# Kernel tuning notes

Hardware: AMD Instinct MI355X
Metric: run time of the kernel (lower is better)

The kernel has to match this reference:

```python
import jax, jax.numpy as jnp
import numpy as np

K_NEIGHBOURS = 4  # neighbour_num
BN_EPS = 1e-5


def setup_inputs() -> dict:
    key = jax.random.key(0)
    ks = jax.random.split(key, 5)
    B, T, J, C = 32, 243, 17, 256
    std = np.sqrt(2.0 / C).astype(np.float32)
    return {
        "x": jax.random.normal(ks[0], (B, T, J, C), dtype=jnp.float32),
        "W_u": jax.random.normal(ks[1], (C, C), dtype=jnp.float32) * std,
        "b_u": jnp.zeros((C,), dtype=jnp.float32),
        "W_v": jax.random.normal(ks[2], (C, C), dtype=jnp.float32) * std,
        "b_v": jnp.zeros((C,), dtype=jnp.float32),
        "gamma": jnp.ones((T,), dtype=jnp.float32),
        "beta": jnp.zeros((T,), dtype=jnp.float32),
    }


def reference(x, W_u, b_u, W_v, b_v, gamma, beta):
    # temporal-mode GCN with top-k similarity adjacency
    b, t, j, c = x.shape
    xr = jnp.transpose(x, (0, 2, 1, 3)).reshape(b * j, t, c)  # [BJ, T, C]

    # similarity adjacency: keep edges >= k-th largest similarity per row
    sim = jnp.einsum('bnc,bmc->bnm', xr, xr)                  # [BJ, T, T]
    thr = jax.lax.top_k(sim, K_NEIGHBOURS)[0][..., -1:]       # [BJ, T, 1]
    adj = (sim >= thr).astype(x.dtype)

    # symmetric degree normalization D^{-1/2} A D^{-1/2}
    deg_inv_sqrt = adj.sum(-1) ** -0.5                        # [BJ, T]
    norm_adj = deg_inv_sqrt[:, :, None] * adj * deg_inv_sqrt[:, None, :]

    v = xr @ W_v.T + b_v
    u = xr @ W_u.T + b_u
    h = jnp.einsum('bnm,bmc->bnc', norm_adj, v) + u           # [BJ, T, C]

    # BatchNorm1d(num_features=T), training mode: stats over (batch, C)
    mean = h.mean(axis=(0, 2), keepdims=True)
    var = jnp.mean((h - mean) ** 2, axis=(0, 2), keepdims=True)
    hn = (h - mean) * jax.lax.rsqrt(var + BN_EPS) * gamma[None, :, None] + beta[None, :, None]

    out = jax.nn.relu(xr + hn)                                # residual (dim_in == dim_out)
    return jnp.transpose(out.reshape(b, j, t, c), (0, 2, 1, 3))  # [B, T, J, C]
```

## Files before the change

### kernel.cpp

```cpp
#include <hip/hip_runtime.h>

#define BB 32
#define TT 243
#define JJ 17
#define CC 256
#define BJC (BB*JJ)
#define MM (BJC*TT)
#define FR (BJC*256)
#define SIMP 244
#define NEG_INF (-3.0e38f)

typedef __attribute__((ext_vector_type(8))) short bf16x8;
typedef __attribute__((ext_vector_type(4))) float f32x4;
typedef __attribute__((ext_vector_type(8))) _Float16 f16x8;
typedef __attribute__((ext_vector_type(4))) _Float16 f16x4;

__device__ __forceinline__ unsigned short f2bf(float f) {
  unsigned int u = __float_as_uint(f);
  u = (u + 0x7fffu + ((u >> 16) & 1u)) >> 16;
  return (unsigned short)u;
}
__device__ __forceinline__ float bf2f(unsigned short s) {
  return __uint_as_float(((unsigned int)s) << 16);
}

__device__ __forceinline__ void gld16(const void* g, void* l) {
  __builtin_amdgcn_global_load_lds(
      (__attribute__((address_space(1))) void*)(g),
      (__attribute__((address_space(3))) void*)(l), 16, 0, 0);
}

__launch_bounds__(256)
__global__ void k_prep_w(const float* __restrict__ Wu, const float* __restrict__ Wv,
                         _Float16* __restrict__ wcp) {
  const int r = blockIdx.x * 4 + (threadIdx.x >> 6);
  const int l = threadIdx.x & 63;
  const float* src = ((r < CC) ? (Wu + (size_t)r * CC) : (Wv + (size_t)(r - CC) * CC)) + l * 4;
  float4 v = *reinterpret_cast<const float4*>(src);
  f16x4 hv = (f16x4){(_Float16)v.x, (_Float16)v.y, (_Float16)v.z, (_Float16)v.w};
  const int ks = l >> 4;
  const int u  = (l & 15) >> 1;
  const int s  = u ^ (r & 7);
  *reinterpret_cast<f16x4*>(wcp + ((size_t)ks * 512 + r) * 64 + s * 8 + (l & 1) * 4) = hv;
}

__launch_bounds__(256)
__global__ void k_prep_x(const float* __restrict__ x,
                         _Float16* __restrict__ xqh, _Float16* __restrict__ xql) {
  const int r = blockIdx.x * 4 + (threadIdx.x >> 6);
  const int l = threadIdx.x & 63;
  const int bj = r / TT, t = r - bj * TT;
  const int b = bj / JJ, j = bj - b * JJ;
  float4 v = *reinterpret_cast<const float4*>(
      x + ((size_t)(b * TT + t) * JJ + j) * CC + l * 4);
  _Float16 h0 = (_Float16)v.x, h1 = (_Float16)v.y, h2 = (_Float16)v.z, h3 = (_Float16)v.w;
  f16x4 hv = (f16x4){h0, h1, h2, h3};
  f16x4 lv = (f16x4){(_Float16)(v.x - (float)h0), (_Float16)(v.y - (float)h1),
                     (_Float16)(v.z - (float)h2), (_Float16)(v.w - (float)h3)};
  const int fr = bj * 256 + t;
  const int ks = l >> 4;
  const int u  = (l & 15) >> 1;
  const int s  = u ^ (t & 7);
  const size_t off = ((size_t)ks * FR + fr) * 64 + s * 8 + (l & 1) * 4;
  *reinterpret_cast<f16x4*>(xqh + off) = hv;
  *reinterpret_cast<f16x4*>(xql + off) = lv;
}

__launch_bounds__(512, 4)
__global__ void k_sim(const _Float16* __restrict__ xqh, const _Float16* __restrict__ xql,
                      float* __restrict__ sim) {
  __shared__ _Float16 Sh[256 * 64];
  __shared__ _Float16 Sl[256 * 64];
  const int bid = blockIdx.x;
  const int g = bid >> 4, s_ = bid & 15;
  const int bj = g * 8 + (s_ & 7);
  const int rh = s_ >> 3;
  const int tid = threadIdx.x, lane = tid & 63, wid = tid >> 6;
  const int wr = wid >> 2, wc = wid & 3;
  const int rowbase = rh * 128 + wr * 64;
  const int l15 = lane & 15, lg = lane >> 4;
  const size_t rb = (size_t)bj * 256;
  const size_t lsrc = (size_t)(lane >> 3) * 64 + (lane & 7) * 8;

  f32x4 acc[4][4];
  #pragma unroll
  for (int i = 0; i < 4; i++)
    #pragma unroll
    for (int j = 0; j < 4; j++) acc[i][j] = (f32x4){0.f, 0.f, 0.f, 0.f};

  for (int ks = 0; ks < 4; ++ks) {
    {
      const _Float16* ph = xqh + ((size_t)ks * FR + rb) * 64;
      const _Float16* pl = xql + ((size_t)ks * FR + rb) * 64;
      #pragma unroll
      for (int c = 0; c < 4; ++c) {
        const int row0 = (wid * 4 + c) * 8;
        gld16(ph + (size_t)row0 * 64 + lsrc, &Sh[row0 * 64]);
        gld16(pl + (size_t)row0 * 64 + lsrc, &Sl[row0 * 64]);
      }
    }
    __syncthreads();
    #pragma unroll
    for (int kh = 0; kh < 2; ++kh) {
      f16x8 bhv[4], blv[4];
      #pragma unroll
      for (int j = 0; j < 4; ++j) {
        int rc = wc * 64 + j * 16 + l15;
        int sl = ((kh * 4 + lg) ^ (rc & 7)) * 8;
        bhv[j] = *reinterpret_cast<const f16x8*>(&Sh[rc * 64 + sl]);
        blv[j] = *reinterpret_cast<const f16x8*>(&Sl[rc * 64 + sl]);
      }
      #pragma unroll
      for (int i = 0; i < 4; ++i) {
        int rl = rowbase + i * 16 + l15;
        int sl = ((kh * 4 + lg) ^ (rl & 7)) * 8;
        f16x8 ah = *reinterpret_cast<const f16x8*>(&Sh[rl * 64 + sl]);
        f16x8 al = *reinterpret_cast<const f16x8*>(&Sl[rl * 64 + sl]);
        #pragma unroll
        for (int j = 0; j < 4; ++j) {
          acc[i][j] = __builtin_amdgcn_mfma_f32_16x16x32_f16(ah, bhv[j], acc[i][j], 0, 0, 0);
          acc[i][j] = __builtin_amdgcn_mfma_f32_16x16x32_f16(ah, blv[j], acc[i][j], 0, 0, 0);
          acc[i][j] = __builtin_amdgcn_mfma_f32_16x16x32_f16(al, bhv[j], acc[i][j], 0, 0, 0);
        }
      }
    }
    if (ks < 3) __syncthreads();
  }

  const size_t sbase = (size_t)bj * TT * SIMP;
  #pragma unroll
  for (int j = 0; j < 4; ++j) {
    int c = wc * 64 + j * 16 + l15;
    if (c < TT) {
      #pragma unroll
      for (int i = 0; i < 4; ++i) {
        int n0 = rowbase + i * 16 + lg * 4;
        if (n0 + 3 < TT) {
          *reinterpret_cast<float4*>(sim + sbase + (size_t)c * SIMP + n0) =
            (float4){acc[i][j][0], acc[i][j][1], acc[i][j][2], acc[i][j][3]};
        } else {
          #pragma unroll
          for (int q = 0; q < 4; ++q)
            if (n0 + q < TT) sim[sbase + (size_t)c * SIMP + n0 + q] = acc[i][j][q];
        }
      }
    }
  }
}

__launch_bounds__(256)
__global__ void k_uv(const _Float16* __restrict__ xqh, const _Float16* __restrict__ wcp,
                     const float* __restrict__ bu, const float* __restrict__ bv,
                     unsigned short* __restrict__ uo, unsigned short* __restrict__ vo) {
  __shared__ _Float16 S[2][128][64];
  const int bid = blockIdx.x;
  const int g = bid >> 5, s_ = bid & 31;
  const int panel = g * 8 + (s_ & 7);
  const int ct = s_ >> 3;
  const int m0 = panel * 128;
  const int tid = threadIdx.x, lane = tid & 63, wid = tid >> 6;
  const int rm = wid * 32;
  const int l15 = lane & 15, lg = lane >> 4;

  const float* bsrc = (ct < 2) ? bu : bv;
  unsigned short* osrc = (ct < 2) ? uo : vo;
  const int cb = (ct & 1) * 128;

  float bias[8];
  #pragma unroll
  for (int j = 0; j < 8; ++j) bias[j] = bsrc[cb + j * 16 + l15];

  f32x4 acc[2][8];
  #pragma unroll
  for (int i = 0; i < 2; i++)
    #pragma unroll
    for (int j = 0; j < 8; j++) acc[i][j] = (f32x4){0.f, 0.f, 0.f, 0.f};

  for (int ks = 0; ks < 4; ++ks) {
    #pragma unroll
    for (int c = 0; c < 8; ++c) {
      int ch = wid * 8 + c;
      int half = ch >> 4;
      int rows0 = (ch & 15) * 8;
      const _Float16* g2 = half
        ? wcp + ((size_t)ks * 512 + ct * 128 + rows0) * 64 + lane * 8
        : xqh + ((size_t)ks * FR  + m0       + rows0) * 64 + lane * 8;
      gld16(g2, &S[half][rows0][0]);
    }
    __syncthreads();
    #pragma unroll
    for (int kh = 0; kh < 2; ++kh) {
      f16x8 af[2], bfv[8];
      #pragma unroll
      for (int i = 0; i < 2; ++i) {
        int rl = rm + i * 16 + l15;
        af[i] = *reinterpret_cast<const f16x8*>(&S[0][rl][((kh * 4 + lg) ^ (rl & 7)) * 8]);
      }
      #pragma unroll
      for (int j = 0; j < 8; ++j) {
        int rl = j * 16 + l15;
        bfv[j] = *reinterpret_cast<const f16x8*>(&S[1][rl][((kh * 4 + lg) ^ (rl & 7)) * 8]);
      }
      #pragma unroll
      for (int i = 0; i < 2; ++i)
        #pragma unroll
        for (int j = 0; j < 8; ++j)
          acc[i][j] = __builtin_amdgcn_mfma_f32_16x16x32_f16(af[i], bfv[j], acc[i][j], 0, 0, 0);
    }
    __syncthreads();
  }

  #pragma unroll
  for (int i = 0; i < 2; ++i) {
    #pragma unroll
    for (int q = 0; q < 4; ++q) {
      int gf = m0 + rm + i * 16 + lg * 4 + q;
      int t = gf & 255, bj = gf >> 8;
      if (t < TT) {
        size_t gm = (size_t)bj * TT + t;
        #pragma unroll
        for (int j = 0; j < 8; ++j)
          osrc[gm * CC + cb + j * 16 + l15] = f2bf(acc[i][j][q] + bias[j]);
      }
    }
  }
}

__launch_bounds__(256)
__global__ void k_topk(const float* __restrict__ sim,
                       float* __restrict__ dis_o,
                       unsigned long long* __restrict__ mask_o,
                       unsigned char* __restrict__ nbr_o,
                       unsigned char* __restrict__ deg_o) {
  const int l = threadIdx.x & 63, wv = threadIdx.x >> 6;
  const int r = blockIdx.x * 4 + wv;
  const float* row = sim + (size_t)r * SIMP;
  float o0 = row[l];
  float o1 = row[l + 64];
  float o2 = row[l + 128];
  float o3 = (l + 192 < TT) ? row[l + 192] : NEG_INF;
  float v0 = o0, v1 = o1, v2 = o2, v3 = o3;
  { float mx, mn;
    mx=fmaxf(v0,v1); mn=fminf(v0,v1); v0=mx; v1=mn;
    mx=fmaxf(v2,v3); mn=fminf(v2,v3); v2=mx; v3=mn;
    mx=fmaxf(v0,v2); mn=fminf(v0,v2); v0=mx; v2=mn;
    mx=fmaxf(v1,v3); mn=fminf(v1,v3); v1=mx; v3=mn;
    mx=fmaxf(v1,v2); mn=fminf(v1,v2); v1=mx; v2=mn; }
  #pragma unroll
  for (int off = 1; off < 64; off <<= 1) {
    float b0 = __shfl_xor(v0, off), b1 = __shfl_xor(v1, off),
          b2 = __shfl_xor(v2, off), b3 = __shfl_xor(v3, off);
    float t0 = fmaxf(v0, b3), t1 = fmaxf(v1, b2),
          t2 = fmaxf(v2, b1), t3 = fmaxf(v3, b0);
    float mx, mn;
    mx=fmaxf(t0,t2); mn=fminf(t0,t2); t0=mx; t2=mn;
    mx=fmaxf(t1,t3); mn=fminf(t1,t3); t1=mx; t3=mn;
    mx=fmaxf(t0,t1); mn=fminf(t0,t1); t0=mx; t1=mn;
    mx=fmaxf(t2,t3); mn=fminf(t2,t3); t2=mx; t3=mn;
    v0=t0; v1=t1; v2=t2; v3=t3;
  }
  const float thr = v3;

  unsigned long long m0 = __ballot(o0 >= thr);
  unsigned long long m1 = __ballot(o1 >= thr);
  unsigned long long m2 = __ballot(o2 >= thr);
  unsigned long long m3 = __ballot(o3 >= thr);
  const unsigned long long below = (1ull << l) - 1ull;
  const int b0 = __popcll(m0);
  const int b1 = b0 + __popcll(m1);
  const int b2 = b1 + __popcll(m2);
  const size_t r8 = (size_t)r * 8;
  if (o0 >= thr) { int q = __popcll(m0 & below);      if (q < 8) nbr_o[r8 + q] = (unsigned char)l; }
  if (o1 >= thr) { int q = b0 + __popcll(m1 & below); if (q < 8) nbr_o[r8 + q] = (unsigned char)(64 + l); }
  if (o2 >= thr) { int q = b1 + __popcll(m2 & below); if (q < 8) nbr_o[r8 + q] = (unsigned char)(128 + l); }
  if (o3 >= thr) { int q = b2 + __popcll(m3 & below); if (q < 8) nbr_o[r8 + q] = (unsigned char)(192 + l); }
  if (l == 0) {
    int deg = b2 + __popcll(m3);
    dis_o[r] = rsqrtf((float)deg);
    deg_o[r] = (unsigned char)((deg > 255) ? 255 : deg);
    mask_o[(size_t)r * 4 + 0] = m0;
    mask_o[(size_t)r * 4 + 1] = m1;
    mask_o[(size_t)r * 4 + 2] = m2;
    mask_o[(size_t)r * 4 + 3] = m3;
  }
}

__launch_bounds__(512)
__global__ void k_agg(const unsigned char* __restrict__ nbr,
                      const unsigned char* __restrict__ degv,
                      const unsigned long long* __restrict__ mask,
                      const float* __restrict__ dis,
                      const unsigned short* __restrict__ u,
                      const unsigned short* __restrict__ v,
                      unsigned short* __restrict__ h,
                      float* __restrict__ p1, float* __restrict__ p2) {
  __shared__ float dis_l[256];
  const int bj = blockIdx.x;
  const int tid = threadIdx.x, lane = tid & 63, wid = tid >> 6;
  if (tid < TT) dis_l[tid] = dis[(size_t)bj * TT + tid];
  __syncthreads();
  const int start = blockIdx.y * 122;
  const int cnt = blockIdx.y ? (TT - 122) : 122;
  const size_t pbase = (size_t)bj * TT;
  const int co = lane * 4;
  for (int rl = wid; rl < cnt; rl += 8) {
    const int t = start + rl;
    const size_t r = pbase + t;
    const float dr = dis_l[t];
    const int dg = degv[r];
    const unsigned long long nb = *reinterpret_cast<const unsigned long long*>(nbr + r * 8);
    ushort4 uu = *reinterpret_cast<const ushort4*>(u + r * CC + co);
    float a0 = bf2f(uu.x), a1 = bf2f(uu.y), a2 = bf2f(uu.z), a3 = bf2f(uu.w);
    if (dg <= 8) {
      const int i0 = (int)(nb & 255), i1 = (int)((nb >> 8) & 255),
                i2 = (int)((nb >> 16) & 255), i3 = (int)((nb >> 24) & 255);
      ushort4 w0v = *reinterpret_cast<const ushort4*>(v + (pbase + i0) * CC + co);
      ushort4 w1v = *reinterpret_cast<const ushort4*>(v + (pbase + i1) * CC + co);
      ushort4 w2v = *reinterpret_cast<const ushort4*>(v + (pbase + i2) * CC + co);
      ushort4 w3v = *reinterpret_cast<const ushort4*>(v + (pbase + i3) * CC + co);
      const float w0 = dr * dis_l[i0], w1 = dr * dis_l[i1],
                  w2 = dr * dis_l[i2], w3 = dr * dis_l[i3];
      a0 = __builtin_fmaf(w0, bf2f(w0v.x), a0); a1 = __builtin_fmaf(w0, bf2f(w0v.y), a1);
      a2 = __builtin_fmaf(w0, bf2f(w0v.z), a2); a3 = __builtin_fmaf(w0, bf2f(w0v.w), a3);
      a0 = __builtin_fmaf(w1, bf2f(w1v.x), a0); a1 = __builtin_fmaf(w1, bf2f(w1v.y), a1);
      a2 = __builtin_fmaf(w1, bf2f(w1v.z), a2); a3 = __builtin_fmaf(w1, bf2f(w1v.w), a3);
      a0 = __builtin_fmaf(w2, bf2f(w2v.x), a0); a1 = __builtin_fmaf(w2, bf2f(w2v.y), a1);
      a2 = __builtin_fmaf(w2, bf2f(w2v.z), a2); a3 = __builtin_fmaf(w2, bf2f(w2v.w), a3);
      a0 = __builtin_fmaf(w3, bf2f(w3v.x), a0); a1 = __builtin_fmaf(w3, bf2f(w3v.y), a1);
      a2 = __builtin_fmaf(w3, bf2f(w3v.z), a2); a3 = __builtin_fmaf(w3, bf2f(w3v.w), a3);
      #pragma unroll
      for (int e = 4; e < 8; ++e) {
        if (e < dg) {
          const int ix = (int)((nb >> (8 * e)) & 255);
          const float we = dr * dis_l[ix];
          ushort4 vv = *reinterpret_cast<const ushort4*>(v + (pbase + ix) * CC + co);
          a0 = __builtin_fmaf(we, bf2f(vv.x), a0); a1 = __builtin_fmaf(we, bf2f(vv.y), a1);
          a2 = __builtin_fmaf(we, bf2f(vv.z), a2); a3 = __builtin_fmaf(we, bf2f(vv.w), a3);
        }
      }
    } else {
      #pragma unroll
      for (int w4 = 0; w4 < 4; ++w4) {
        unsigned long long m = mask[r * 4 + w4];
        while (m) {
          int i = __ffsll(m) - 1;
          m &= m - 1;
          int idx = w4 * 64 + i;
          float w = dr * dis_l[idx];
          ushort4 vv = *reinterpret_cast<const ushort4*>(v + (pbase + idx) * CC + co);
          a0 = __builtin_fmaf(w, bf2f(vv.x), a0);
          a1 = __builtin_fmaf(w, bf2f(vv.y), a1);
          a2 = __builtin_fmaf(w, bf2f(vv.z), a2);
          a3 = __builtin_fmaf(w, bf2f(vv.w), a3);
        }
      }
    }
    ushort4 hh;
    hh.x = f2bf(a0); hh.y = f2bf(a1); hh.z = f2bf(a2); hh.w = f2bf(a3);
    *reinterpret_cast<ushort4*>(h + r * CC + co) = hh;
    float s1 = a0 + a1 + a2 + a3;
    float s2 = a0*a0 + a1*a1 + a2*a2 + a3*a3;
    #pragma unroll
    for (int off = 1; off < 64; off <<= 1) { s1 += __shfl_xor(s1, off); s2 += __shfl_xor(s2, off); }
    if (lane == 0) { p1[r] = s1; p2[r] = s2; }
  }
}

__global__ void k_bnstat(const float* __restrict__ p1, const float* __restrict__ p2,
                         const float* __restrict__ gamma, const float* __restrict__ beta,
                         float* __restrict__ scale, float* __restrict__ shift) {
  __shared__ float sA[256], sB[256];
  const int t = blockIdx.x;
  const int tid = threadIdx.x;
  float a = 0.f, b2 = 0.f;
  for (int bj = tid; bj < BJC; bj += 256) {
    a  += p1[bj * TT + t];
    b2 += p2[bj * TT + t];
  }
  sA[tid] = a; sB[tid] = b2;
  __syncthreads();
  for (int s = 128; s > 0; s >>= 1) {
    if (tid < s) { sA[tid] += sA[tid + s]; sB[tid] += sB[tid + s]; }
    __syncthreads();
  }
  if (tid == 0) {
    const float invN = 1.0f / (float)(BJC * CC);
    float mean = sA[0] * invN;
    float var  = sB[0] * invN - mean * mean;
    float sc   = rsqrtf(var + 1e-5f) * gamma[t];
    scale[t] = sc;
    shift[t] = beta[t] - mean * sc;
  }
}

__global__ void k_out(const float* __restrict__ x, const unsigned short* __restrict__ h,
                      const float* __restrict__ scale, const float* __restrict__ shift,
                      float* __restrict__ out) {
  int g = blockIdx.x * 256 + threadIdx.x;
  if (g >= MM * (CC/4)) return;
  int c4  = g & 63;
  int rowx = g >> 6;
  int b   = rowx / (TT*JJ);
  int rem = rowx - b*(TT*JJ);
  int t   = rem / JJ;
  int j   = rem - t*JJ;
  size_t hoff = ((size_t)(b*JJ + j) * TT + t) * CC + c4*4;
  float4 xv = *reinterpret_cast<const float4*>(x + (size_t)rowx*CC + c4*4);
  ushort4 hv = *reinterpret_cast<const ushort4*>(h + hoff);
  float sc = scale[t], sh = shift[t];
  float4 o;
  o.x = fmaxf(xv.x + bf2f(hv.x)*sc + sh, 0.f);
  o.y = fmaxf(xv.y + bf2f(hv.y)*sc + sh, 0.f);
  o.z = fmaxf(xv.z + bf2f(hv.z)*sc + sh, 0.f);
  o.w = fmaxf(xv.w + bf2f(hv.w)*sc + sh, 0.f);
  *reinterpret_cast<float4*>(out + (size_t)rowx*CC + c4*4) = o;
}

extern "C" void kernel_launch(void* const* d_in, const int* in_sizes, int n_in,
                              void* d_out, int out_size, void* d_ws, size_t ws_size,
                              hipStream_t stream) {
  const float* x     = (const float*)d_in[0];
  const float* Wu    = (const float*)d_in[1];
  const float* bu    = (const float*)d_in[2];
  const float* Wv    = (const float*)d_in[3];
  const float* bv    = (const float*)d_in[4];
  const float* gamma = (const float*)d_in[5];
  const float* beta  = (const float*)d_in[6];
  float* out = (float*)d_out;

  char* ws = (char*)d_ws;
  size_t off = 0;
  auto alloc = [&](size_t bytes) -> void* {
    void* p = ws + off;
    off = (off + bytes + 255) & ~(size_t)255;
    return p;
  };
  _Float16* xqh = (_Float16*)alloc((size_t)4 * FR * 64 * 2);
  _Float16* xql = (_Float16*)alloc((size_t)4 * FR * 64 * 2);
  _Float16* wcp = (_Float16*)alloc((size_t)4 * 512 * 64 * 2);
  float* sim = (float*)alloc((size_t)BJC * TT * SIMP * 4);
  float* dis = (float*)alloc((size_t)MM * 4);
  unsigned long long* msk = (unsigned long long*)alloc((size_t)MM * 4 * 8);
  unsigned char* nbr = (unsigned char*)alloc((size_t)MM * 8);
  unsigned char* deg = (unsigned char*)alloc((size_t)MM);
  float* p1    = (float*)alloc((size_t)MM * 4);
  float* p2    = (float*)alloc((size_t)MM * 4);
  float* scale = (float*)alloc(1024);
  float* shift = (float*)alloc(1024);
  unsigned short* v = (unsigned short*)alloc((size_t)MM * CC * 2);
  unsigned short* u = (unsigned short*)sim;
  unsigned short* h = (unsigned short*)xql;

  if (ws_size < off) {
    hipMemsetAsync(d_out, 0, (size_t)out_size * 4, stream);
    return;
  }

  k_prep_w<<<dim3(512/4), dim3(256), 0, stream>>>(Wu, Wv, wcp);
  k_prep_x<<<dim3(MM/4), dim3(256), 0, stream>>>(x, xqh, xql);
  k_sim  <<<dim3(BJC*2), dim3(512), 0, stream>>>(xqh, xql, sim);
  k_topk <<<dim3(MM/4), dim3(256), 0, stream>>>(sim, dis, msk, nbr, deg);
  k_uv   <<<dim3(4*(FR/128)), dim3(256), 0, stream>>>(xqh, wcp, bu, bv, u, v);
  k_agg  <<<dim3(BJC, 2), dim3(512), 0, stream>>>(nbr, deg, msk, dis, u, v, h, p1, p2);
  k_bnstat<<<dim3(TT), dim3(256), 0, stream>>>(p1, p2, gamma, beta, scale, shift);
  k_out  <<<dim3((MM*(CC/4) + 255)/256), dim3(256), 0, stream>>>(x, h, scale, shift, out);
}
```

Measured before the change: 393.2 us.

## Merge similarity and U/V GEMM kernels into one launch

Combines the sim GEMM and the U/V projection GEMM into one kernel that picks its role from the block index, so the two independent GEMMs share a single launch and can overlap on the GPU. The U/V part now runs 512-thread blocks that each compute a full 256-column output for either U or V, reusing one loaded A tile across twice as many columns. U gets its own workspace buffer instead of aliasing the sim buffer, which costs extra memory traffic and footprint. The shared 64KB LDS allocation and 512-thread blocks may limit occupancy for the U/V role.

```diff
diff --git a/kernel.cpp b/kernel.cpp
--- a/kernel.cpp
+++ b/kernel.cpp
@@ -9,6 +9,8 @@
 #define FR (BJC*256)
 #define SIMP 244
 #define NEG_INF (-3.0e38f)
+#define NSIMB (BJC*2)
+#define NUVB  (FR/128*2)
 
 typedef __attribute__((ext_vector_type(8))) short bf16x8;
 typedef __attribute__((ext_vector_type(4))) float f32x4;
@@ -67,160 +69,164 @@
 }
 
 __launch_bounds__(512, 4)
-__global__ void k_sim(const _Float16* __restrict__ xqh, const _Float16* __restrict__ xql,
-                      float* __restrict__ sim) {
-  __shared__ _Float16 Sh[256 * 64];
-  __shared__ _Float16 Sl[256 * 64];
-  const int bid = blockIdx.x;
-  const int g = bid >> 4, s_ = bid & 15;
-  const int bj = g * 8 + (s_ & 7);
-  const int rh = s_ >> 3;
+__global__ void k_main(const _Float16* __restrict__ xqh, const _Float16* __restrict__ xql,
+                       const _Float16* __restrict__ wcp,
+                       const float* __restrict__ bu, const float* __restrict__ bv,
+                       float* __restrict__ sim,
+                       unsigned short* __restrict__ uo, unsigned short* __restrict__ vo) {
+  __shared__ __align__(16) char LB[65536];
   const int tid = threadIdx.x, lane = tid & 63, wid = tid >> 6;
-  const int wr = wid >> 2, wc = wid & 3;
-  const int rowbase = rh * 128 + wr * 64;
   const int l15 = lane & 15, lg = lane >> 4;
-  const size_t rb = (size_t)bj * 256;
   const size_t lsrc = (size_t)(lane >> 3) * 64 + (lane & 7) * 8;
 
-  f32x4 acc[4][4];
-  #pragma unroll
-  for (int i = 0; i < 4; i++)
+  if (blockIdx.x < NSIMB) {
+    _Float16* Sh = (_Float16*)LB;
+    _Float16* Sl = (_Float16*)(LB + 32768);
+    const int bid = blockIdx.x;
+    const int g = bid >> 4, s_ = bid & 15;
+    const int bj = g * 8 + (s_ & 7);
+    const int rh = s_ >> 3;
+    const int wr = wid >> 2, wc = wid & 3;
+    const int rowbase = rh * 128 + wr * 64;
+    const size_t rb = (size_t)bj * 256;
+
+    f32x4 acc[4][4];
     #pragma unroll
-    for (int j = 0; j < 4; j++) acc[i][j] = (f32x4){0.f, 0.f, 0.f, 0.f};
-
-  for (int ks = 0; ks < 4; ++ks) {
-    {
-      const _Float16* ph = xqh + ((size_t)ks * FR + rb) * 64;
-      const _Float16* pl = xql + ((size_t)ks * FR + rb) * 64;
-      #pragma unroll
-      for (int c = 0; c < 4; ++c) {
-        const int row0 = (wid * 4 + c) * 8;
-        gld16(ph + (size_t)row0 * 64 + lsrc, &Sh[row0 * 64]);
-        gld16(pl + (size_t)row0 * 64 + lsrc, &Sl[row0 * 64]);
-      }
+    for (int i = 0; i < 4; i++)
+      #pragma unroll
+      for (int j = 0; j < 4; j++) acc[i][j] = (f32x4){0.f, 0.f, 0.f, 0.f};
+
+    for (int ks = 0; ks < 4; ++ks) {
+      {
+        const _Float16* ph = xqh + ((size_t)ks * FR + rb) * 64;
+        const _Float16* pl = xql + ((size_t)ks * FR + rb) * 64;
+        #pragma unroll
+        for (int c = 0; c < 4; ++c) {
+          const int row0 = (wid * 4 + c) * 8;
+          gld16(ph + (size_t)row0 * 64 + lsrc, Sh + row0 * 64);
+          gld16(pl + (size_t)row0 * 64 + lsrc, Sl + row0 * 64);
+        }
+      }
+      __syncthreads();
+      #pragma unroll
+      for (int kh = 0; kh < 2; ++kh) {
+        f16x8 bhv[4], blv[4];
+        #pragma unroll
+        for (int j = 0; j < 4; ++j) {
+          int rc = wc * 64 + j * 16 + l15;
+          int sl = ((kh * 4 + lg) ^ (rc & 7)) * 8;
+          bhv[j] = *reinterpret_cast<const f16x8*>(&Sh[rc * 64 + sl]);
+          blv[j] = *reinterpret_cast<const f16x8*>(&Sl[rc * 64 + sl]);
+        }
+        #pragma unroll
+        for (int i = 0; i < 4; ++i) {
+          int rl = rowbase + i * 16 + l15;
+          int sl = ((kh * 4 + lg) ^ (rl & 7)) * 8;
+          f16x8 ah = *reinterpret_cast<const f16x8*>(&Sh[rl * 64 + sl]);
+          f16x8 al = *reinterpret_cast<const f16x8*>(&Sl[rl * 64 + sl]);
+          #pragma unroll
+          for (int j = 0; j < 4; ++j) {
+            acc[i][j] = __builtin_amdgcn_mfma_f32_16x16x32_f16(ah, bhv[j], acc[i][j], 0, 0, 0);
+            acc[i][j] = __builtin_amdgcn_mfma_f32_16x16x32_f16(ah, blv[j], acc[i][j], 0, 0, 0);
+            acc[i][j] = __builtin_amdgcn_mfma_f32_16x16x32_f16(al, bhv[j], acc[i][j], 0, 0, 0);
+          }
+        }
+      }
+      if (ks < 3) __syncthreads();
     }
-    __syncthreads();
+
+    const size_t sbase = (size_t)bj * TT * SIMP;
     #pragma unroll
-    for (int kh = 0; kh < 2; ++kh) {
-      f16x8 bhv[4], blv[4];
-      #pragma unroll
-      for (int j = 0; j < 4; ++j) {
-        int rc = wc * 64 + j * 16 + l15;
-        int sl = ((kh * 4 + lg) ^ (rc & 7)) * 8;
-        bhv[j] = *reinterpret_cast<const f16x8*>(&Sh[rc * 64 + sl]);
-        blv[j] = *reinterpret_cast<const f16x8*>(&Sl[rc * 64 + sl]);
-      }
-      #pragma unroll
-      for (int i = 0; i < 4; ++i) {
-        int rl = rowbase + i * 16 + l15;
-        int sl = ((kh * 4 + lg) ^ (rl & 7)) * 8;
-        f16x8 ah = *reinterpret_cast<const f16x8*>(&Sh[rl * 64 + sl]);
-        f16x8 al = *reinterpret_cast<const f16x8*>(&Sl[rl * 64 + sl]);
-        #pragma unroll
-        for (int j = 0; j < 4; ++j) {
-          acc[i][j] = __builtin_amdgcn_mfma_f32_16x16x32_f16(ah, bhv[j], acc[i][j], 0, 0, 0);
-          acc[i][j] = __builtin_amdgcn_mfma_f32_16x16x32_f16(ah, blv[j], acc[i][j], 0, 0, 0);
-          acc[i][j] = __builtin_amdgcn_mfma_f32_16x16x32_f16(al, bhv[j], acc[i][j], 0, 0, 0);
+    for (int j = 0; j < 4; ++j) {
+      int c = wc * 64 + j * 16 + l15;
+      if (c < TT) {
+        #pragma unroll
+        for (int i = 0; i < 4; ++i) {
+          int n0 = rowbase + i * 16 + lg * 4;
+          if (n0 + 3 < TT) {
+            *reinterpret_cast<float4*>(sim + sbase + (size_t)c * SIMP + n0) =
+              (float4){acc[i][j][0], acc[i][j][1], acc[i][j][2], acc[i][j][3]};
+          } else {
+            #pragma unroll
+            for (int q = 0; q < 4; ++q)
+              if (n0 + q < TT) sim[sbase + (size_t)c * SIMP + n0 + q] = acc[i][j][q];
+          }
         }
       }
     }
-    if (ks < 3) __syncthreads();
-  }
-
-  const size_t sbase = (size_t)bj * TT * SIMP;
-  #pragma unroll
-  for (int j = 0; j < 4; ++j) {
-    int c = wc * 64 + j * 16 + l15;
-    if (c < TT) {
-      #pragma unroll
-      for (int i = 0; i < 4; ++i) {
-        int n0 = rowbase + i * 16 + lg * 4;
-        if (n0 + 3 < TT) {
-          *reinterpret_cast<float4*>(sim + sbase + (size_t)c * SIMP + n0) =
-            (float4){acc[i][j][0], acc[i][j][1], acc[i][j][2], acc[i][j][3]};
+  } else {
+    _Float16* As = (_Float16*)LB;
+    _Float16* Bs = (_Float16*)(LB + 16384);
+    const int bid2 = blockIdx.x - NSIMB;
+    const int cu = bid2 & 1;
+    const int panel = bid2 >> 1;
+    const int m0 = panel * 128;
+    const int rm = (wid & 3) * 32;
+    const int ch = wid >> 2;
+
+    const float* bsrc = cu ? bv : bu;
+    unsigned short* osrc = cu ? vo : uo;
+
+    f32x4 acc[2][8];
+    #pragma unroll
+    for (int i = 0; i < 2; i++)
+      #pragma unroll
+      for (int j = 0; j < 8; j++) acc[i][j] = (f32x4){0.f, 0.f, 0.f, 0.f};
+
+    for (int ks = 0; ks < 4; ++ks) {
+      #pragma unroll
+      for (int c = 0; c < 6; ++c) {
+        int chk = wid * 6 + c;
+        if (chk < 16) {
+          int row0 = chk * 8;
+          gld16(xqh + ((size_t)ks * FR + m0 + row0) * 64 + lsrc, As + row0 * 64);
         } else {
+          int row0 = (chk - 16) * 8;
+          gld16(wcp + ((size_t)ks * 512 + cu * 256 + row0) * 64 + lsrc, Bs + row0 * 64);
+        }
+      }
+      __syncthreads();
+      #pragma unroll
+      for (int kh = 0; kh < 2; ++kh) {
+        f16x8 af[2];
+        #pragma unroll
+        for (int i = 0; i < 2; ++i) {
+          int rl = rm + i * 16 + l15;
+          af[i] = *reinterpret_cast<const f16x8*>(&As[rl * 64 + ((kh * 4 + lg) ^ (rl & 7)) * 8]);
+        }
+        #pragma unroll
+        for (int jh = 0; jh < 2; ++jh) {
+          f16x8 bfv[4];
           #pragma unroll
-          for (int q = 0; q < 4; ++q)
-            if (n0 + q < TT) sim[sbase + (size_t)c * SIMP + n0 + q] = acc[i][j][q];
-        }
-      }
+          for (int j = 0; j < 4; ++j) {
+            int rb2 = ch * 128 + jh * 64 + j * 16 + l15;
+            bfv[j] = *reinterpret_cast<const f16x8*>(&Bs[rb2 * 64 + ((kh * 4 + lg) ^ (rb2 & 7)) * 8]);
+          }
+          #pragma unroll
+          for (int i = 0; i < 2; ++i)
+            #pragma unroll
+            for (int j = 0; j < 4; ++j)
+              acc[i][jh * 4 + j] =
+                __builtin_amdgcn_mfma_f32_16x16x32_f16(af[i], bfv[j], acc[i][jh * 4 + j], 0, 0, 0);
+        }
+      }
+      if (ks < 3) __syncthreads();
     }
-  }
-}
-
-__launch_bounds__(256)
-__global__ void k_uv(const _Float16* __restrict__ xqh, const _Float16* __restrict__ wcp,
-                     const float* __restrict__ bu, const float* __restrict__ bv,
-                     unsigned short* __restrict__ uo, unsigned short* __restrict__ vo) {
-  __shared__ _Float16 S[2][128][64];
-  const int bid = blockIdx.x;
-  const int g = bid >> 5, s_ = bid & 31;
-  const int panel = g * 8 + (s_ & 7);
-  const int ct = s_ >> 3;
-  const int m0 = panel * 128;
-  const int tid = threadIdx.x, lane = tid & 63, wid = tid >> 6;
-  const int rm = wid * 32;
-  const int l15 = lane & 15, lg = lane >> 4;
-
-  const float* bsrc = (ct < 2) ? bu : bv;
-  unsigned short* osrc = (ct < 2) ? uo : vo;
-  const int cb = (ct & 1) * 128;
-
-  float bias[8];
-  #pragma unroll
-  for (int j = 0; j < 8; ++j) bias[j] = bsrc[cb + j * 16 + l15];
-
-  f32x4 acc[2][8];
-  #pragma unroll
-  for (int i = 0; i < 2; i++)
+
     #pragma unroll
-    for (int j = 0; j < 8; j++) acc[i][j] = (f32x4){0.f, 0.f, 0.f, 0.f};
-
-  for (int ks = 0; ks < 4; ++ks) {
-    #pragma unroll
-    for (int c = 0; c < 8; ++c) {
-      int ch = wid * 8 + c;
-      int half = ch >> 4;
-      int rows0 = (ch & 15) * 8;
-      const _Float16* g2 = half
-        ? wcp + ((size_t)ks * 512 + ct * 128 + rows0) * 64 + lane * 8
-        : xqh + ((size_t)ks * FR  + m0       + rows0) * 64 + lane * 8;
-      gld16(g2, &S[half][rows0][0]);
-    }
-    __syncthreads();
-    #pragma unroll
-    for (int kh = 0; kh < 2; ++kh) {
-      f16x8 af[2], bfv[8];
-      #pragma unroll
-      for (int i = 0; i < 2; ++i) {
-        int rl = rm + i * 16 + l15;
-        af[i] = *reinterpret_cast<const f16x8*>(&S[0][rl][((kh * 4 + lg) ^ (rl & 7)) * 8]);
-      }
-      #pragma unroll
-      for (int j = 0; j < 8; ++j) {
-        int rl = j * 16 + l15;
-        bfv[j] = *reinterpret_cast<const f16x8*>(&S[1][rl][((kh * 4 + lg) ^ (rl & 7)) * 8]);
-      }
-      #pragma unroll
-      for (int i = 0; i < 2; ++i)
-        #pragma unroll
-        for (int j = 0; j < 8; ++j)
-          acc[i][j] = __builtin_amdgcn_mfma_f32_16x16x32_f16(af[i], bfv[j], acc[i][j], 0, 0, 0);
-    }
-    __syncthreads();
-  }
-
-  #pragma unroll
-  for (int i = 0; i < 2; ++i) {
-    #pragma unroll
-    for (int q = 0; q < 4; ++q) {
-      int gf = m0 + rm + i * 16 + lg * 4 + q;
-      int t = gf & 255, bj = gf >> 8;
-      if (t < TT) {
-        size_t gm = (size_t)bj * TT + t;
-        #pragma unroll
-        for (int j = 0; j < 8; ++j)
-          osrc[gm * CC + cb + j * 16 + l15] = f2bf(acc[i][j][q] + bias[j]);
+    for (int i = 0; i < 2; ++i) {
+      #pragma unroll
+      for (int q = 0; q < 4; ++q) {
+        int gf = m0 + rm + i * 16 + lg * 4 + q;
+        int t = gf & 255, bj = gf >> 8;
+        if (t < TT) {
+          size_t gm = (size_t)bj * TT + t;
+          #pragma unroll
+          for (int j = 0; j < 8; ++j) {
+            int col = ch * 128 + j * 16 + l15;
+            osrc[gm * CC + col] = f2bf(acc[i][j][q] + bsrc[col]);
+          }
+        }
       }
     }
   }
@@ -447,8 +453,8 @@
   float* p2    = (float*)alloc((size_t)MM * 4);
   float* scale = (float*)alloc(1024);
   float* shift = (float*)alloc(1024);
+  unsigned short* u = (unsigned short*)alloc((size_t)MM * CC * 2);
   unsigned short* v = (unsigned short*)alloc((size_t)MM * CC * 2);
-  unsigned short* u = (unsigned short*)sim;
   unsigned short* h = (unsigned short*)xql;
 
   if (ws_size < off) {
@@ -458,9 +464,8 @@
 
   k_prep_w<<<dim3(512/4), dim3(256), 0, stream>>>(Wu, Wv, wcp);
   k_prep_x<<<dim3(MM/4), dim3(256), 0, stream>>>(x, xqh, xql);
-  k_sim  <<<dim3(BJC*2), dim3(512), 0, stream>>>(xqh, xql, sim);
+  k_main <<<dim3(NSIMB + NUVB), dim3(512), 0, stream>>>(xqh, xql, wcp, bu, bv, sim, u, v);
   k_topk <<<dim3(MM/4), dim3(256), 0, stream>>>(sim, dis, msk, nbr, deg);
-  k_uv   <<<dim3(4*(FR/128)), dim3(256), 0, stream>>>(xqh, wcp, bu, bv, u, v);
   k_agg  <<<dim3(BJC, 2), dim3(512), 0, stream>>>(nbr, deg, msk, dis, u, v, h, p1, p2);
   k_bnstat<<<dim3(TT), dim3(256), 0, stream>>>(p1, p2, gamma, beta, scale, shift);
   k_out  <<<dim3((MM*(CC/4) + 255)/256), dim3(256), 0, stream>>>(x, h, scale, shift, out);
```

Measured after the change: 404.2 us. 1.03x slower.
